# Kernel tuning notes

Hardware: AMD Instinct MI355X
Metric: run time of the kernel (lower is better)

Reference implementation:

```python
import jax, jax.numpy as jnp
import numpy as np

NG, ND, D, H = 50000, 20000, 128, 128
EGG, EGDA, ELAB = 800000, 400000, 200000
EPS, SLOPE = 1e-5, 0.01


def setup_inputs() -> dict:
    key = jax.random.key(0)
    ks = jax.random.split(key, 24)
    w = lambda k, s: jax.random.normal(k, s, jnp.float32) * 0.05
    return {
        "x_gene": jax.random.normal(ks[0], (NG, D), jnp.float32),
        "x_disease": jax.random.normal(ks[1], (ND, D), jnp.float32),
        "W_dst1": w(ks[2], (3, D, H)), "W_src1": w(ks[3], (3, D, H)),
        "W_upd1": w(ks[4], (3, 2 * H, H)),
        "b_dst1": w(ks[5], (3, H)), "b_src1": w(ks[6], (3, H)), "b_upd1": w(ks[7], (3, H)),
        "W_dst2": w(ks[8], (3, H, H)), "W_src2": w(ks[9], (3, H, H)),
        "W_upd2": w(ks[10], (3, 2 * H, H)),
        "b_dst2": w(ks[11], (3, H)), "b_src2": w(ks[12], (3, H)), "b_upd2": w(ks[13], (3, H)),
        "bn_gamma": jnp.ones((2, H), jnp.float32), "bn_beta": jnp.zeros((2, H), jnp.float32),
        "gg_src": jax.random.randint(ks[14], (EGG,), 0, NG, jnp.int32),
        "gg_dst": jax.random.randint(ks[15], (EGG,), 0, NG, jnp.int32),
        "gda_src": jax.random.randint(ks[16], (EGDA,), 0, NG, jnp.int32),
        "gda_dst": jax.random.randint(ks[17], (EGDA,), 0, ND, jnp.int32),
        "label_src": jax.random.randint(ks[18], (ELAB,), 0, NG, jnp.int32),
        "label_dst": jax.random.randint(ks[19], (ELAB,), 0, ND, jnp.int32),
    }


def _mean_agg(x_src, src_idx, dst_idx, n_dst):
    # matmul(adj_t, x_src, reduce='mean'): per-dst mean of neighbor features (0 if no in-edges)
    s = jax.ops.segment_sum(x_src[src_idx], dst_idx, num_segments=n_dst)
    deg = jax.ops.segment_sum(jnp.ones((src_idx.shape[0],), x_src.dtype), dst_idx, num_segments=n_dst)
    return s / jnp.maximum(deg, 1.0)[:, None]


def _conv(i, x_src, x_dst, src_idx, dst_idx, n_dst, Wd, Ws, Wu, bd, bs, bu):
    agg = _mean_agg(x_src, src_idx, dst_idx, n_dst)
    dst_msg = x_dst @ Wd[i] + bd[i]
    src_msg = agg @ Ws[i] + bs[i]
    return jnp.concatenate([dst_msg, src_msg], axis=1) @ Wu[i] + bu[i]


def _layer(xg, xd, Wd, Ws, Wu, bd, bs, bu, gg_src, gg_dst, gda_src, gda_dst):
    out_gg = _conv(0, xg, xg, gg_src, gg_dst, NG, Wd, Ws, Wu, bd, bs, bu)    # gene -> gene
    out_gda = _conv(1, xg, xd, gda_src, gda_dst, ND, Wd, Ws, Wu, bd, bs, bu)  # gene -> disease
    out_rev = _conv(2, xd, xg, gda_dst, gda_src, NG, Wd, Ws, Wu, bd, bs, bu)  # disease -> gene (reverse edges)
    gene = 0.5 * (out_gg + out_rev)  # stack+mean across edge types for gene dst
    return gene, out_gda


def _bn(x, g, b):
    # BatchNorm1d in training mode: batch stats over node dim, biased variance
    m = jnp.mean(x, axis=0)
    v = jnp.mean((x - m) ** 2, axis=0)
    return (x - m) * jax.lax.rsqrt(v + EPS) * g + b


def _lrelu(x):
    return jnp.where(x >= 0, x, SLOPE * x)


def reference(x_gene, x_disease, W_dst1, W_src1, W_upd1, b_dst1, b_src1, b_upd1,
              W_dst2, W_src2, W_upd2, b_dst2, b_src2, b_upd2, bn_gamma, bn_beta,
              gg_src, gg_dst, gda_src, gda_dst, label_src, label_dst):
    g, d = _layer(x_gene, x_disease, W_dst1, W_src1, W_upd1, b_dst1, b_src1, b_upd1,
                  gg_src, gg_dst, gda_src, gda_dst)
    g = _lrelu(_bn(g, bn_gamma[0], bn_beta[0]))
    d = _lrelu(_bn(d, bn_gamma[1], bn_beta[1]))
    g, d = _layer(g, d, W_dst2, W_src2, W_upd2, b_dst2, b_src2, b_upd2,
                  gg_src, gg_dst, gda_src, gda_dst)
    # dot-product decoder on supervision (gene, gda, disease) label edges
    return jnp.sum(g[label_src] * d[label_dst], axis=-1)
```

## Files before the change

### kernel.cpp

```cpp
#include <hip/hip_runtime.h>
#include <hip/hip_bf16.h>
#include <cstddef>

#define NG   50000
#define ND   20000
#define DH   128
#define EGG  800000
#define EGDA 400000
#define ELAB 200000

#define B1G 391
#define B1D 157
#define TB  939
#define TBP 940
#define PB0 0
#define PB1 (NG+1)
#define PB2 (NG+1+ND+1)

typedef __hip_bfloat16  bf16;
typedef __attribute__((ext_vector_type(8))) short bf16x8;
typedef __attribute__((ext_vector_type(4))) float f32x4;
typedef __attribute__((ext_vector_type(2))) float f32x2;

__device__ __forceinline__ float bf2f(short s){
  return __uint_as_float(((unsigned)(unsigned short)s) << 16);
}
__device__ __forceinline__ unsigned short f2b(float x){
  unsigned u = __float_as_uint(x);
  return (unsigned short)((u + 0x7FFF + ((u >> 16) & 1)) >> 16);
}

__device__ __forceinline__ float fp8_dec1(unsigned v){
  unsigned s = (v >> 7) & 1, e = (v >> 3) & 15, m = v & 7;
  float r = e ? __uint_as_float(((e + 120) << 23) | (m << 20))
              : (float)m * 0.001953125f;
  return s ? -r : r;
}
__device__ __forceinline__ unsigned fp8_enc1(float x){
  float a = fabsf(x);
  if (a > 448.f) a = 448.f;
  unsigned sgn = (__float_as_uint(x) >> 31) << 7;
  unsigned res;
  if (a < 0.015625f){
    res = (unsigned)__float2int_rn(a * 512.f);
    if (res > 7) res = 8;
    if (res == 8) res = 0x08;
  } else {
    unsigned ab = __float_as_uint(a);
    unsigned r = ab + 0x0007FFFF + ((ab >> 20) & 1);
    int e = (int)(r >> 23) - 127;
    unsigned m = (r >> 20) & 7;
    if (e > 8){ e = 8; m = 6; }
    res = ((unsigned)(e + 7) << 3) | m;
  }
  return res | sgn;
}

__device__ __forceinline__ void fp8x4_acc(unsigned w, float* a){
#if __has_builtin(__builtin_amdgcn_cvt_pk_f32_fp8)
  f32x2 p0 = __builtin_amdgcn_cvt_pk_f32_fp8((int)w, false);
  f32x2 p1 = __builtin_amdgcn_cvt_pk_f32_fp8((int)w, true);
  a[0] += p0.x; a[1] += p0.y; a[2] += p1.x; a[3] += p1.y;
#else
  a[0] += fp8_dec1(w & 255);
  a[1] += fp8_dec1((w >> 8) & 255);
  a[2] += fp8_dec1((w >> 16) & 255);
  a[3] += fp8_dec1(w >> 24);
#endif
}
__device__ __forceinline__ unsigned fp8x4_enc(float x0, float x1, float x2, float x3){
#if __has_builtin(__builtin_amdgcn_cvt_pk_fp8_f32)
  int v = 0;
  v = __builtin_amdgcn_cvt_pk_fp8_f32(x0, x1, v, false);
  v = __builtin_amdgcn_cvt_pk_fp8_f32(x2, x3, v, true);
  return (unsigned)v;
#else
  return fp8_enc1(x0) | (fp8_enc1(x1) << 8) | (fp8_enc1(x2) << 16) | (fp8_enc1(x3) << 24);
#endif
}

__global__ __launch_bounds__(256) void k_hist1(const int* __restrict__ k0, const int* __restrict__ k1,
                                               const int* __restrict__ k2, int* __restrict__ hist){
  __shared__ int lh[400];
  const int g = blockIdx.y;
  const int n  = (g == 0) ? EGG : EGDA;
  const int B1 = (g == 1) ? B1D : B1G;
  const int bb = (g == 0) ? 0 : (g == 1 ? B1G : B1G + B1D);
  const int* key = (g == 0) ? k0 : (g == 1 ? k1 : k2);
  for (int t = threadIdx.x; t < B1; t += 256) lh[t] = 0;
  __syncthreads();
  for (int i = blockIdx.x*blockDim.x + threadIdx.x; i < n; i += gridDim.x*blockDim.x)
    atomicAdd(&lh[key[i] >> 7], 1);
  __syncthreads();
  for (int t = threadIdx.x; t < B1; t += 256){
    int c = lh[t];
    if (c) atomicAdd(&hist[bb + t], c);
  }
}

__global__ __launch_bounds__(1024) void k_exscan(const int* __restrict__ cnt,
                                                 int* __restrict__ ptr, int* __restrict__ cur, int n){
  __shared__ int wsum[16];
  __shared__ int carry;
  const int tid = threadIdx.x, lane = tid & 63, wid = tid >> 6;
  if (tid == 0) carry = 0;
  __syncthreads();
  for (int base = 0; base < n; base += 4096){
    int i0 = base + tid*4;
    int4 v = {0,0,0,0};
    if (i0 < n) v = *(const int4*)(cnt + i0);
    int tsum = v.x + v.y + v.z + v.w;
    int x = tsum;
    #pragma unroll
    for (int off = 1; off < 64; off <<= 1){
      int t = __shfl_up(x, off);
      if (lane >= off) x += t;
    }
    if (lane == 63) wsum[wid] = x;
    __syncthreads();
    if (wid == 0 && lane < 16){
      int w = wsum[lane];
      #pragma unroll
      for (int off = 1; off < 16; off <<= 1){
        int t = __shfl_up(w, off);
        if (lane >= off) w += t;
      }
      wsum[lane] = w;
    }
    __syncthreads();
    int waveoff = wid ? wsum[wid-1] : 0;
    if (i0 < n){
      int ex = carry + waveoff + x - tsum;
      int4 o;
      o.x = ex; o.y = ex + v.x; o.z = o.y + v.y; o.w = o.z + v.z;
      *(int4*)(ptr + i0) = o;
      *(int4*)(cur + i0) = o;
    }
    int total = wsum[15];
    __syncthreads();
    if (tid == 0) carry += total;
    __syncthreads();
  }
  if (tid == 0) ptr[n] = carry;
}

__global__ __launch_bounds__(256) void k_scatter1(const int* __restrict__ k0, const int* __restrict__ v0,
                                                  const int* __restrict__ k1, const int* __restrict__ v1,
                                                  int* __restrict__ gcur, unsigned* __restrict__ pk){
  __shared__ int lh[400];
  __shared__ int base[400];
  const int g = blockIdx.y;
  const int n  = (g == 0) ? EGG : EGDA;
  const int B1 = (g == 1) ? B1D : B1G;
  const int bb = (g == 0) ? 0 : (g == 1 ? B1G : B1G + B1D);
  const int* key = (g == 0) ? k0 : (g == 1 ? k1 : v1);
  const int* val = (g == 0) ? v0 : (g == 1 ? v1 : k1);
  const int tid = threadIdx.x;
  const int chunk0 = blockIdx.x*4096;
  if (chunk0 >= n) return;
  for (int t = tid; t < B1; t += 256) lh[t] = 0;
  __syncthreads();
  int kd[16], vv[16];
  #pragma unroll
  for (int it = 0; it < 16; ++it){
    int i = chunk0 + it*256 + tid;
    int k = -1, v = 0;
    if (i < n){ k = key[i]; v = val[i]; atomicAdd(&lh[k >> 7], 1); }
    kd[it] = k; vv[it] = v;
  }
  __syncthreads();
  for (int t = tid; t < B1; t += 256){
    int c = lh[t];
    base[t] = c ? atomicAdd(&gcur[bb + t], c) : 0;
    lh[t] = 0;
  }
  __syncthreads();
  #pragma unroll
  for (int it = 0; it < 16; ++it){
    int k = kd[it];
    if (k >= 0){
      int b = k >> 7;
      int p = base[b] + atomicAdd(&lh[b], 1);
      pk[p] = ((unsigned)(k & 127) << 17) | (unsigned)vv[it];
    }
  }
}

__global__ __launch_bounds__(256) void k_csr2(const unsigned* __restrict__ pk,
                                              const int* __restrict__ gbase,
                                              int* __restrict__ ptr_all, int* __restrict__ col){
  __shared__ int lh[128];
  __shared__ int cur[128];
  __shared__ int sh0;
  const int b = blockIdx.x, tid = threadIdx.x;
  int lb, pbase, Ngr, bend;
  if (b < B1G)            { lb = b;             pbase = PB0; Ngr = NG; bend = B1G; }
  else if (b < B1G + B1D) { lb = b - B1G;       pbase = PB1; Ngr = ND; bend = B1G + B1D; }
  else                    { lb = b - B1G - B1D; pbase = PB2; Ngr = NG; bend = TB; }
  const int s = gbase[b], e = gbase[b+1];
  if (tid < 128) lh[tid] = 0;
  __syncthreads();
  for (int i = s + tid; i < e; i += 256)
    atomicAdd(&lh[(pk[i] >> 17) & 127], 1);
  __syncthreads();
  int lane = tid & 63;
  int v = 0, x = 0;
  if (tid < 128){
    v = lh[tid]; x = v;
    #pragma unroll
    for (int o = 1; o < 64; o <<= 1){
      int t = __shfl_up(x, o);
      if (lane >= o) x += t;
    }
    if (tid == 63) sh0 = x;
  }
  __syncthreads();
  if (tid < 128){
    int excl = x - v + (tid >= 64 ? sh0 : 0);
    cur[tid] = s + excl;
    int loc = (lb << 7) + tid;
    if (loc < Ngr) ptr_all[pbase + loc] = s + excl;
  }
  __syncthreads();
  for (int i = s + tid; i < e; i += 256){
    unsigned p = pk[i];
    int dl = (p >> 17) & 127;
    int pos = atomicAdd(&cur[dl], 1);
    col[pos] = (int)(p & 0x1FFFFu);
  }
  if (lb == 0 && tid == 0) ptr_all[pbase + Ngr] = gbase[bend];
}

#define PREP_F2B_BLOCKS (((NG+ND)*32)/256)
__global__ __launch_bounds__(256) void k_prep(
    const float* __restrict__ Wd1, const float* __restrict__ Ws1, const float* __restrict__ Wu1,
    const float* __restrict__ Wd2, const float* __restrict__ Ws2, const float* __restrict__ Wu2,
    const float* __restrict__ bd1, const float* __restrict__ bs1, const float* __restrict__ bu1,
    const float* __restrict__ bd2, const float* __restrict__ bs2, const float* __restrict__ bu2,
    float* __restrict__ AB, float* __restrict__ cv,
    const float* __restrict__ Xg, const float* __restrict__ Xd,
    unsigned short* __restrict__ Yg, unsigned short* __restrict__ Yd,
    unsigned* __restrict__ Yg8, unsigned* __restrict__ Yd8){
  const int b = blockIdx.x, tid = threadIdx.x;
  if (b < 768){
    int idx = b*256 + tid;
    int layer = idx / 98304;
    int r0 = idx - layer*98304;
    int mat = r0 >> 14;
    int r   = (r0 >> 7) & 127;
    int c   = r0 & 127;
    int i   = mat >> 1;
    int isB = mat & 1;
    const float* Wd = layer ? Wd2 : Wd1;
    const float* Ws = layer ? Ws2 : Ws1;
    const float* Wu = layer ? Wu2 : Wu1;
    const float* P = (isB ? Ws : Wd) + i*16384 + r*128;
    const float* Q = Wu + i*32768 + (isB ? 16384 : 0) + c;
    float s = 0.f;
    for (int h = 0; h < 128; ++h) s += P[h] * Q[h*128];
    AB[idx] = s;
  } else if (b < 771){
    int idx = (b - 768)*256 + tid;
    if (idx >= 768) return;
    int layer = idx / 384;
    int r = idx - layer*384;
    int i = r >> 7, h = r & 127;
    const float* bd = layer ? bd2 : bd1;
    const float* bs = layer ? bs2 : bs1;
    const float* bu = layer ? bu2 : bu1;
    const float* Wu = layer ? Wu2 : Wu1;
    float s = bu[i*128 + h];
    const float* Ut = Wu + i*32768 + h;
    const float* Ub = Ut + 16384;
    for (int k = 0; k < 128; ++k)
      s += bd[i*128 + k] * Ut[k*128] + bs[i*128 + k] * Ub[k*128];
    cv[idx] = s;
  } else {
    int idx = (b - 771)*256 + tid;
    const int GQ = NG*32;
    const float* X; unsigned short* Y; unsigned* Y8; int i;
    if (idx < GQ){ X = Xg; Y = Yg; Y8 = Yg8; i = idx; }
    else         { X = Xd; Y = Yd; Y8 = Yd8; i = idx - GQ; }
    float4 v = ((const float4*)X)[i];
    ushort4 o;
    o.x = f2b(v.x); o.y = f2b(v.y); o.z = f2b(v.z); o.w = f2b(v.w);
    ((ushort4*)Y)[i] = o;
    Y8[i] = fp8x4_enc(v.x, v.y, v.z, v.w);
  }
}

__global__ __launch_bounds__(256) void k_pack(const float* __restrict__ AB, const float* __restrict__ cv,
                                              bf16* __restrict__ Wg1, bf16* __restrict__ Wd1p,
                                              bf16* __restrict__ Wg2, bf16* __restrict__ Wd2p,
                                              float* __restrict__ cg1, float* __restrict__ cd1,
                                              float* __restrict__ cg2, float* __restrict__ cd2){
  int idx = blockIdx.x*256 + threadIdx.x;
  int layer = idx / 81920;
  int rem = idx - layer*81920;
  const float* ABl = AB + layer*98304;
  const float* cvl = cv + layer*384;
  if (rem < 49152){
    int n0  = rem / 6144;
    int r2  = rem - n0*6144;
    int ks  = r2 >> 9;
    int lane = (r2 >> 3) & 63;
    int j   = r2 & 7;
    int k   = ks*32 + (lane >> 4)*8 + j;
    int c   = n0*16 + (lane & 15);
    float v;
    if      (k < 128) v = 0.5f*(ABl[0*16384 + k*128 + c] + ABl[4*16384 + k*128 + c]);
    else if (k < 256) v = 0.5f* ABl[1*16384 + (k-128)*128 + c];
    else              v = 0.5f* ABl[5*16384 + (k-256)*128 + c];
    bf16* W = layer ? Wg2 : Wg1;
    ((unsigned short*)W)[rem] = f2b(v);
    if (rem < 128){
      float* cg = layer ? cg2 : cg1;
      cg[rem] = 0.5f*(cvl[rem] + cvl[256 + rem]);
    }
  } else {
    int d = rem - 49152;
    int n0  = d >> 12;
    int ks  = (d >> 9) & 7;
    int lane = (d >> 3) & 63;
    int j   = d & 7;
    int k   = ks*32 + (lane >> 4)*8 + j;
    int c   = n0*16 + (lane & 15);
    float v = (k < 128) ? ABl[2*16384 + k*128 + c] : ABl[3*16384 + (k-128)*128 + c];
    bf16* W = layer ? Wd2p : Wd1p;
    ((unsigned short*)W)[d] = f2b(v);
    if (d < 128){
      float* cd = layer ? cd2 : cd1;
      cd[d] = cvl[128 + d];
    }
  }
}

__global__ __launch_bounds__(256) void k_agg(const unsigned* __restrict__ Xg8, const unsigned* __restrict__ Xd8,
    const int* __restrict__ ptr_all, const int* __restrict__ col,
    bf16* __restrict__ OutGG, bf16* __restrict__ OutGDA, bf16* __restrict__ OutREV){
  int q = (blockIdx.x*256 + threadIdx.x) >> 4;
  int lane = threadIdx.x & 15;
  const unsigned* X; bf16* Out; const int* ptr; int dst;
  if (q < NG)          { X = Xg8; Out = OutGG;  ptr = ptr_all + PB0; dst = q; }
  else if (q < NG+ND)  { X = Xg8; Out = OutGDA; ptr = ptr_all + PB1; dst = q - NG; }
  else                 { X = Xd8; Out = OutREV; ptr = ptr_all + PB2; dst = q - NG - ND; }
  int s = ptr[dst], e = ptr[dst+1];
  float a[8];
  #pragma unroll
  for (int j = 0; j < 8; ++j) a[j] = 0.f;
  const int loff = lane*2;
  int i = s;
  for (; i + 4 <= e; i += 4){
    uint2 u0 = *(const uint2*)(X + (size_t)col[i  ]*32 + loff);
    uint2 u1 = *(const uint2*)(X + (size_t)col[i+1]*32 + loff);
    uint2 u2 = *(const uint2*)(X + (size_t)col[i+2]*32 + loff);
    uint2 u3 = *(const uint2*)(X + (size_t)col[i+3]*32 + loff);
    fp8x4_acc(u0.x, a);     fp8x4_acc(u0.y, a+4);
    fp8x4_acc(u1.x, a);     fp8x4_acc(u1.y, a+4);
    fp8x4_acc(u2.x, a);     fp8x4_acc(u2.y, a+4);
    fp8x4_acc(u3.x, a);     fp8x4_acc(u3.y, a+4);
  }
  for (; i < e; ++i){
    uint2 u = *(const uint2*)(X + (size_t)col[i]*32 + loff);
    fp8x4_acc(u.x, a);      fp8x4_acc(u.y, a+4);
  }
  float inv = 1.f / fmaxf((float)(e - s), 1.f);
  bf16x8 o;
  #pragma unroll
  for (int j = 0; j < 8; ++j) o[j] = (short)f2b(a[j]*inv);
  *(bf16x8*)(Out + (size_t)dst*DH + (size_t)lane*8) = o;
}

template<int KS>
__device__ __forceinline__ void gemm_body(
    const bf16* __restrict__ X0, const bf16* __restrict__ X1, const bf16* __restrict__ X2,
    const bf16* __restrict__ Wp, const float* __restrict__ cvec,
    unsigned short* __restrict__ Out, int M, int blk){
  const int tid = threadIdx.x;
  const int wave = tid >> 6, lane = tid & 63;
  const int lrow = lane & 15, quad = lane >> 4;
  const int row0 = blk*32;
  const bf16* Xs[3] = {X0, X1, X2};
  f32x4 acc[2][2];
  #pragma unroll
  for (int p = 0; p < 2; ++p)
    #pragma unroll
    for (int t = 0; t < 2; ++t) acc[p][t] = 0.0f;
  const bf16x8* wp = (const bf16x8*)Wp;
  const int f00 = (2*wave*KS)*64 + lane;
  #pragma unroll
  for (int ks = 0; ks < KS; ++ks){
    const bf16* Xm = Xs[ks >> 2];
    const int kk = (ks & 3)*32 + quad*8;
    bf16x8 a[2];
    #pragma unroll
    for (int t = 0; t < 2; ++t){
      int ar = row0 + t*16 + lrow; if (ar > M-1) ar = M-1;
      a[t] = *(const bf16x8*)(Xm + (size_t)ar*DH + kk);
    }
    bf16x8 b0 = wp[f00 + ks*64];
    bf16x8 b1 = wp[f00 + (KS + ks)*64];
    #pragma unroll
    for (int t = 0; t < 2; ++t){
      acc[0][t] = __builtin_amdgcn_mfma_f32_16x16x32_bf16(a[t], b0, acc[0][t], 0, 0, 0);
      acc[1][t] = __builtin_amdgcn_mfma_f32_16x16x32_bf16(a[t], b1, acc[1][t], 0, 0, 0);
    }
  }
  #pragma unroll
  for (int p = 0; p < 2; ++p){
    int c = (2*wave + p)*16 + lrow;
    float cb = cvec[c];
    #pragma unroll
    for (int t = 0; t < 2; ++t){
      #pragma unroll
      for (int r = 0; r < 4; ++r){
        int row = row0 + t*16 + quad*4 + r;
        if (row < M) Out[(size_t)row*DH + c] = f2b(acc[p][t][r] + cb);
      }
    }
  }
}

#define GBGENE ((NG+31)/32)
#define GBDIS  ((ND+31)/32)

__global__ __launch_bounds__(256) void k_gemm(
    const bf16* __restrict__ Xg, const bf16* __restrict__ Ag, const bf16* __restrict__ Rg,
    const bf16* __restrict__ Wg, const float* __restrict__ cg, unsigned short* __restrict__ Og,
    const bf16* __restrict__ Xd, const bf16* __restrict__ Ad,
    const bf16* __restrict__ Wd, const float* __restrict__ cd, unsigned short* __restrict__ Od){
  if ((int)blockIdx.x < GBGENE)
    gemm_body<12>(Xg, Ag, Rg, Wg, cg, Og, NG, blockIdx.x);
  else
    gemm_body<8>(Xd, Ad, Ad, Wd, cd, Od, ND, blockIdx.x - GBGENE);
}

#define SBG 192
#define SBD 64
__global__ __launch_bounds__(256) void k_bn_stats(const bf16* __restrict__ Xgb, const bf16* __restrict__ Xdb,
                                                  float* __restrict__ sums){
  __shared__ float acc[256];
  int tid = threadIdx.x;
  acc[tid] = 0.f;
  __syncthreads();
  int g = (int)blockIdx.x >= SBG;
  int bidx = blockIdx.x - (g ? SBG : 0);
  int NB = g ? SBD : SBG;
  int N  = g ? ND : NG;
  const bf16* Xb = g ? Xdb : Xgb;
  float* sm = sums + g*256;
  int c8 = (tid & 15)*8;
  int rl = tid >> 4;
  float s[8], q[8];
  #pragma unroll
  for (int j = 0; j < 8; ++j){ s[j] = 0.f; q[j] = 0.f; }
  for (int r = bidx*16 + rl; r < N; r += NB*16){
    bf16x8 v = *(const bf16x8*)(Xb + (size_t)r*DH + c8);
    #pragma unroll
    for (int j = 0; j < 8; ++j){
      float f = bf2f(v[j]);
      s[j] += f; q[j] += f*f;
    }
  }
  #pragma unroll
  for (int j = 0; j < 8; ++j){
    atomicAdd(&acc[c8+j], s[j]);
    atomicAdd(&acc[128+c8+j], q[j]);
  }
  __syncthreads();
  atomicAdd(&sm[tid], acc[tid]);
}

__global__ __launch_bounds__(256) void k_bn_apply(const bf16* __restrict__ Xgb, const bf16* __restrict__ Xdb,
    const float* __restrict__ sums, const float* __restrict__ gamma, const float* __restrict__ beta,
    unsigned short* __restrict__ Yg, unsigned short* __restrict__ Yd,
    uint2* __restrict__ Yg8, uint2* __restrict__ Yd8){
  __shared__ float sc[256], sb[256];
  int tid = threadIdx.x;
  {
    int g = tid >> 7, c = tid & 127;
    float invN = g ? (1.f/ND) : (1.f/NG);
    const float* sm = sums + g*256;
    float m = sm[c]*invN;
    float v = sm[128 + c]*invN - m*m;
    float s = rsqrtf(v + 1e-5f) * gamma[g*128 + c];
    sc[tid] = s;
    sb[tid] = beta[g*128 + c] - m*s;
  }
  __syncthreads();
  const int GT = NG*16;
  const int TOT = GT + ND*16;
  for (int idx = blockIdx.x*256 + tid; idx < TOT; idx += gridDim.x*256){
    const bf16x8* src; bf16x8* dst; uint2* dst8; int i, cb;
    if (idx < GT){ src = (const bf16x8*)Xgb; dst = (bf16x8*)Yg; dst8 = Yg8; i = idx; cb = 0; }
    else         { src = (const bf16x8*)Xdb; dst = (bf16x8*)Yd; dst8 = Yd8; i = idx - GT; cb = 128; }
    bf16x8 v = src[i];
    int c = cb + (i & 15)*8;
    float y[8];
    bf16x8 o;
    #pragma unroll
    for (int j = 0; j < 8; ++j){
      float t = bf2f(v[j])*sc[c+j] + sb[c+j];
      t = t >= 0.f ? t : 0.01f*t;
      y[j] = t;
      o[j] = (short)f2b(t);
    }
    dst[i] = o;
    uint2 p;
    p.x = fp8x4_enc(y[0], y[1], y[2], y[3]);
    p.y = fp8x4_enc(y[4], y[5], y[6], y[7]);
    dst8[i] = p;
  }
}

__global__ __launch_bounds__(256) void k_decode(const bf16* __restrict__ G, const bf16* __restrict__ Dd,
    const int* __restrict__ ls, const int* __restrict__ ld, float* __restrict__ out, int E){
  int p = (blockIdx.x*256 + threadIdx.x) >> 4;
  int lane = threadIdx.x & 15;
  int e0 = p*2, e1 = p*2 + 1;
  if (e0 >= E) return;
  int a0 = ls[e0], b0 = ld[e0];
  int a1 = ls[e1], b1 = ld[e1];
  const size_t loff = (size_t)lane*8;
  bf16x8 g0 = *(const bf16x8*)(G  + (size_t)a0*DH + loff);
  bf16x8 d0 = *(const bf16x8*)(Dd + (size_t)b0*DH + loff);
  bf16x8 g1 = *(const bf16x8*)(G  + (size_t)a1*DH + loff);
  bf16x8 d1 = *(const bf16x8*)(Dd + (size_t)b1*DH + loff);
  float s0 = 0.f, s1 = 0.f;
  #pragma unroll
  for (int j = 0; j < 8; ++j){
    s0 += bf2f(g0[j])*bf2f(d0[j]);
    s1 += bf2f(g1[j])*bf2f(d1[j]);
  }
  #pragma unroll
  for (int off = 8; off; off >>= 1){
    s0 += __shfl_down(s0, off, 16);
    s1 += __shfl_down(s1, off, 16);
  }
  if (lane == 0){ out[e0] = s0; out[e1] = s1; }
}

extern "C" void kernel_launch(void* const* d_in, const int* in_sizes, int n_in,
                              void* d_out, int out_size, void* d_ws, size_t ws_size,
                              hipStream_t stream){
  const float* x_gene = (const float*)d_in[0];
  const float* x_dis  = (const float*)d_in[1];
  const float* Wd1 = (const float*)d_in[2];
  const float* Ws1 = (const float*)d_in[3];
  const float* Wu1 = (const float*)d_in[4];
  const float* bd1 = (const float*)d_in[5];
  const float* bs1 = (const float*)d_in[6];
  const float* bu1 = (const float*)d_in[7];
  const float* Wd2 = (const float*)d_in[8];
  const float* Ws2 = (const float*)d_in[9];
  const float* Wu2 = (const float*)d_in[10];
  const float* bd2 = (const float*)d_in[11];
  const float* bs2 = (const float*)d_in[12];
  const float* bu2 = (const float*)d_in[13];
  const float* bng = (const float*)d_in[14];
  const float* bnb = (const float*)d_in[15];
  const int* gg_src  = (const int*)d_in[16];
  const int* gg_dst  = (const int*)d_in[17];
  const int* gda_src = (const int*)d_in[18];
  const int* gda_dst = (const int*)d_in[19];
  const int* lsrc = (const int*)d_in[20];
  const int* ldst = (const int*)d_in[21];

  char* ws = (char*)d_ws;
  size_t off = 0;
  auto alloc = [&](size_t bytes)->void*{
    void* p = ws + off; off += (bytes + 255) & ~(size_t)255; return p;
  };
  int* hist    = (int*)alloc(960*4);
  float* bnsum = (float*)alloc(2*256*4);
  int* gbase   = (int*)alloc(960*4);
  int* gcur    = (int*)alloc(960*4);
  int* ptr_all = (int*)alloc((size_t)(NG+1+ND+1+NG+1)*4);
  int* col     = (int*)alloc((size_t)(EGG+2*EGDA)*4);
  unsigned* pk = (unsigned*)alloc((size_t)(EGG+2*EGDA)*4);
  float* AB  = (float*)alloc(2*98304*4);
  float* cv  = (float*)alloc(2*384*4);
  float* cg1 = (float*)alloc(128*4);
  float* cd1 = (float*)alloc(128*4);
  float* cg2 = (float*)alloc(128*4);
  float* cd2 = (float*)alloc(128*4);
  bf16* Wg1  = (bf16*)alloc(49152*2);
  bf16* Wp1  = (bf16*)alloc(32768*2);
  bf16* Wg2  = (bf16*)alloc(49152*2);
  bf16* Wp2  = (bf16*)alloc(32768*2);
  bf16* xgb  = (bf16*)alloc((size_t)NG*DH*2);
  bf16* xdb  = (bf16*)alloc((size_t)ND*DH*2);
  unsigned* xg8  = (unsigned*)alloc((size_t)NG*DH);
  unsigned* xd8  = (unsigned*)alloc((size_t)ND*DH);
  unsigned* Xg28 = (unsigned*)alloc((size_t)NG*DH);
  unsigned* Xd28 = (unsigned*)alloc((size_t)ND*DH);
  bf16* aggGGb  = (bf16*)alloc((size_t)NG*DH*2);
  bf16* aggREVb = (bf16*)alloc((size_t)NG*DH*2);
  bf16* aggGDAb = (bf16*)alloc((size_t)ND*DH*2);
  bf16* Xg2b = (bf16*)alloc((size_t)NG*DH*2);
  bf16* Xd2b = (bf16*)alloc((size_t)ND*DH*2);
  bf16* outgb = (bf16*)alloc((size_t)NG*DH*2);
  bf16* outdb = (bf16*)alloc((size_t)ND*DH*2);

  hipMemsetAsync(hist, 0, 960*4 + 512*4, stream);

  {
    dim3 gh(96, 3);
    k_hist1<<<gh,256,0,stream>>>(gg_dst, gda_dst, gda_src, hist);
    k_exscan<<<1,1024,0,stream>>>(hist, gbase, gcur, TBP);
    dim3 gs(196, 3);
    k_scatter1<<<gs,256,0,stream>>>(gg_dst, gg_src, gda_dst, gda_src, gcur, pk);
    k_csr2<<<TB,256,0,stream>>>(pk, gbase, ptr_all, col);
  }

  k_prep<<<771 + PREP_F2B_BLOCKS,256,0,stream>>>(
      Wd1, Ws1, Wu1, Wd2, Ws2, Wu2, bd1, bs1, bu1, bd2, bs2, bu2,
      AB, cv, x_gene, x_dis, (unsigned short*)xgb, (unsigned short*)xdb, xg8, xd8);
  k_pack<<<640,256,0,stream>>>(AB, cv, Wg1, Wp1, Wg2, Wp2, cg1, cd1, cg2, cd2);

  k_agg<<<(NG+ND+NG)*16/256,256,0,stream>>>(xg8, xd8, ptr_all, col, aggGGb, aggGDAb, aggREVb);
  k_gemm<<<GBGENE+GBDIS,256,0,stream>>>(xgb, aggGGb, aggREVb, Wg1, cg1, (unsigned short*)outgb,
                                        xdb, aggGDAb, Wp1, cd1, (unsigned short*)outdb);
  k_bn_stats<<<SBG+SBD,256,0,stream>>>(outgb, outdb, bnsum);
  k_bn_apply<<<1024,256,0,stream>>>(outgb, outdb, bnsum, bng, bnb,
                                    (unsigned short*)Xg2b, (unsigned short*)Xd2b,
                                    (uint2*)Xg28, (uint2*)Xd28);

  k_agg<<<(NG+ND+NG)*16/256,256,0,stream>>>(Xg28, Xd28, ptr_all, col, aggGGb, aggGDAb, aggREVb);
  k_gemm<<<GBGENE+GBDIS,256,0,stream>>>(Xg2b, aggGGb, aggREVb, Wg2, cg2, (unsigned short*)outgb,
                                        Xd2b, aggGDAb, Wp2, cd2, (unsigned short*)outdb);

  k_decode<<<ELAB*16/2/256,256,0,stream>>>(outgb, outdb, lsrc, ldst, (float*)d_out, ELAB);
}
```

Baseline: 344.4 us.

## Fuse neighbor aggregation and BN statistics into the per-layer GEMM kernel

Merges the aggregation kernel, the GEMM kernel and the BN-statistics kernel into one k_layer kernel. Each 32-row block first gathers mean-aggregated neighbor features into LDS, then runs the MFMA GEMM reading aggregated operands from LDS. In the first layer it also accumulates per-column sum and sum of squares in the epilogue. This removes the global round trip for the aggregation buffers and two kernel launches per layer. In exchange, the gather work is now serialized with the GEMM inside each block, using only 16 row-gathers in flight per block, and every block issues global atomics.

Result: slower. 355.7 us (+3.3%).

```diff
diff --git a/kernel.cpp b/kernel.cpp
--- a/kernel.cpp
+++ b/kernel.cpp
@@ -335,52 +335,63 @@
   }
 }
 
-__global__ __launch_bounds__(256) void k_agg(const unsigned* __restrict__ Xg8, const unsigned* __restrict__ Xd8,
-    const int* __restrict__ ptr_all, const int* __restrict__ col,
-    bf16* __restrict__ OutGG, bf16* __restrict__ OutGDA, bf16* __restrict__ OutREV){
-  int q = (blockIdx.x*256 + threadIdx.x) >> 4;
-  int lane = threadIdx.x & 15;
-  const unsigned* X; bf16* Out; const int* ptr; int dst;
-  if (q < NG)          { X = Xg8; Out = OutGG;  ptr = ptr_all + PB0; dst = q; }
-  else if (q < NG+ND)  { X = Xg8; Out = OutGDA; ptr = ptr_all + PB1; dst = q - NG; }
-  else                 { X = Xd8; Out = OutREV; ptr = ptr_all + PB2; dst = q - NG - ND; }
-  int s = ptr[dst], e = ptr[dst+1];
-  float a[8];
-  #pragma unroll
-  for (int j = 0; j < 8; ++j) a[j] = 0.f;
-  const int loff = lane*2;
-  int i = s;
-  for (; i + 4 <= e; i += 4){
-    uint2 u0 = *(const uint2*)(X + (size_t)col[i  ]*32 + loff);
-    uint2 u1 = *(const uint2*)(X + (size_t)col[i+1]*32 + loff);
-    uint2 u2 = *(const uint2*)(X + (size_t)col[i+2]*32 + loff);
-    uint2 u3 = *(const uint2*)(X + (size_t)col[i+3]*32 + loff);
-    fp8x4_acc(u0.x, a);     fp8x4_acc(u0.y, a+4);
-    fp8x4_acc(u1.x, a);     fp8x4_acc(u1.y, a+4);
-    fp8x4_acc(u2.x, a);     fp8x4_acc(u2.y, a+4);
-    fp8x4_acc(u3.x, a);     fp8x4_acc(u3.y, a+4);
-  }
-  for (; i < e; ++i){
-    uint2 u = *(const uint2*)(X + (size_t)col[i]*32 + loff);
-    fp8x4_acc(u.x, a);      fp8x4_acc(u.y, a+4);
-  }
-  float inv = 1.f / fmaxf((float)(e - s), 1.f);
-  bf16x8 o;
-  #pragma unroll
-  for (int j = 0; j < 8; ++j) o[j] = (short)f2b(a[j]*inv);
-  *(bf16x8*)(Out + (size_t)dst*DH + (size_t)lane*8) = o;
-}
-
-template<int KS>
-__device__ __forceinline__ void gemm_body(
-    const bf16* __restrict__ X0, const bf16* __restrict__ X1, const bf16* __restrict__ X2,
+#define GBG32 ((NG+31)/32)
+#define GBD32 ((ND+31)/32)
+
+template<int KS, int DO_BN>
+__device__ __forceinline__ void layer_body(
+    const bf16* __restrict__ X0,
+    const unsigned* __restrict__ S8a, const unsigned* __restrict__ S8b,
+    const int* __restrict__ ptrA, const int* __restrict__ ptrB,
+    const int* __restrict__ col,
     const bf16* __restrict__ Wp, const float* __restrict__ cvec,
-    unsigned short* __restrict__ Out, int M, int blk){
+    unsigned short* __restrict__ Out, float* __restrict__ bnglob,
+    int M, int blk, short (*lds_agg)[32][128], float* bnacc){
   const int tid = threadIdx.x;
+  const int row0 = blk*32;
+
+  {
+    const int qw = tid >> 4, lane = tid & 15;
+    const int loff = lane*2;
+    const int NT = (KS == 12) ? 64 : 32;
+    for (int t = qw; t < NT; t += 16){
+      int lr  = (KS == 12) ? (t >> 1) : t;
+      int row = row0 + lr;
+      if (row < M){
+        int g = (KS == 12) ? (t & 1) : 0;
+        const unsigned* X8 = g ? S8b : S8a;
+        const int* ptr = g ? ptrB : ptrA;
+        int s = ptr[row], e = ptr[row+1];
+        float a[8];
+        #pragma unroll
+        for (int j = 0; j < 8; ++j) a[j] = 0.f;
+        int i = s;
+        for (; i + 4 <= e; i += 4){
+          uint2 u0 = *(const uint2*)(X8 + (size_t)col[i  ]*32 + loff);
+          uint2 u1 = *(const uint2*)(X8 + (size_t)col[i+1]*32 + loff);
+          uint2 u2 = *(const uint2*)(X8 + (size_t)col[i+2]*32 + loff);
+          uint2 u3 = *(const uint2*)(X8 + (size_t)col[i+3]*32 + loff);
+          fp8x4_acc(u0.x, a);     fp8x4_acc(u0.y, a+4);
+          fp8x4_acc(u1.x, a);     fp8x4_acc(u1.y, a+4);
+          fp8x4_acc(u2.x, a);     fp8x4_acc(u2.y, a+4);
+          fp8x4_acc(u3.x, a);     fp8x4_acc(u3.y, a+4);
+        }
+        for (; i < e; ++i){
+          uint2 u = *(const uint2*)(X8 + (size_t)col[i]*32 + loff);
+          fp8x4_acc(u.x, a);      fp8x4_acc(u.y, a+4);
+        }
+        float inv = 1.f / fmaxf((float)(e - s), 1.f);
+        bf16x8 o;
+        #pragma unroll
+        for (int j = 0; j < 8; ++j) o[j] = (short)f2b(a[j]*inv);
+        *(bf16x8*)&lds_agg[g][lr][lane*8] = o;
+      }
+    }
+  }
+  __syncthreads();
+
   const int wave = tid >> 6, lane = tid & 63;
   const int lrow = lane & 15, quad = lane >> 4;
-  const int row0 = blk*32;
-  const bf16* Xs[3] = {X0, X1, X2};
   f32x4 acc[2][2];
   #pragma unroll
   for (int p = 0; p < 2; ++p)
@@ -390,13 +401,13 @@
   const int f00 = (2*wave*KS)*64 + lane;
   #pragma unroll
   for (int ks = 0; ks < KS; ++ks){
-    const bf16* Xm = Xs[ks >> 2];
     const int kk = (ks & 3)*32 + quad*8;
     bf16x8 a[2];
     #pragma unroll
     for (int t = 0; t < 2; ++t){
       int ar = row0 + t*16 + lrow; if (ar > M-1) ar = M-1;
-      a[t] = *(const bf16x8*)(Xm + (size_t)ar*DH + kk);
+      if (ks < 4) a[t] = *(const bf16x8*)(X0 + (size_t)ar*DH + kk);
+      else        a[t] = *(const bf16x8*)&lds_agg[(ks >> 2) - 1][ar - row0][kk];
     }
     bf16x8 b0 = wp[f00 + ks*64];
     bf16x8 b1 = wp[f00 + (KS + ks)*64];
@@ -406,69 +417,55 @@
       acc[1][t] = __builtin_amdgcn_mfma_f32_16x16x32_bf16(a[t], b1, acc[1][t], 0, 0, 0);
     }
   }
+
   #pragma unroll
   for (int p = 0; p < 2; ++p){
     int c = (2*wave + p)*16 + lrow;
     float cb = cvec[c];
+    float sl = 0.f, ql = 0.f;
     #pragma unroll
     for (int t = 0; t < 2; ++t){
       #pragma unroll
       for (int r = 0; r < 4; ++r){
         int row = row0 + t*16 + quad*4 + r;
-        if (row < M) Out[(size_t)row*DH + c] = f2b(acc[p][t][r] + cb);
+        if (row < M){
+          unsigned short us = f2b(acc[p][t][r] + cb);
+          Out[(size_t)row*DH + c] = us;
+          if (DO_BN){
+            float f = bf2f((short)us);
+            sl += f; ql += f*f;
+          }
+        }
       }
     }
-  }
-}
-
-#define GBGENE ((NG+31)/32)
-#define GBDIS  ((ND+31)/32)
-
-__global__ __launch_bounds__(256) void k_gemm(
-    const bf16* __restrict__ Xg, const bf16* __restrict__ Ag, const bf16* __restrict__ Rg,
+    if (DO_BN){
+      atomicAdd(&bnacc[c], sl);
+      atomicAdd(&bnacc[128 + c], ql);
+    }
+  }
+  if (DO_BN){
+    __syncthreads();
+    atomicAdd(&bnglob[tid], bnacc[tid]);
+  }
+}
+
+template<int DO_BN>
+__global__ __launch_bounds__(256) void k_layer(
+    const bf16* __restrict__ Xg, const bf16* __restrict__ Xd,
+    const unsigned* __restrict__ xg8, const unsigned* __restrict__ xd8,
+    const int* __restrict__ ptr_all, const int* __restrict__ col,
     const bf16* __restrict__ Wg, const float* __restrict__ cg, unsigned short* __restrict__ Og,
-    const bf16* __restrict__ Xd, const bf16* __restrict__ Ad,
-    const bf16* __restrict__ Wd, const float* __restrict__ cd, unsigned short* __restrict__ Od){
-  if ((int)blockIdx.x < GBGENE)
-    gemm_body<12>(Xg, Ag, Rg, Wg, cg, Og, NG, blockIdx.x);
+    const bf16* __restrict__ Wd, const float* __restrict__ cd, unsigned short* __restrict__ Od,
+    float* __restrict__ bnsum){
+  __shared__ short lds_agg[2][32][128];
+  __shared__ float bnacc[256];
+  if (DO_BN) bnacc[threadIdx.x] = 0.f;
+  if ((int)blockIdx.x < GBG32)
+    layer_body<12, DO_BN>(Xg, xg8, xd8, ptr_all + PB0, ptr_all + PB2, col,
+                          Wg, cg, Og, bnsum, NG, blockIdx.x, lds_agg, bnacc);
   else
-    gemm_body<8>(Xd, Ad, Ad, Wd, cd, Od, ND, blockIdx.x - GBGENE);
-}
-
-#define SBG 192
-#define SBD 64
-__global__ __launch_bounds__(256) void k_bn_stats(const bf16* __restrict__ Xgb, const bf16* __restrict__ Xdb,
-                                                  float* __restrict__ sums){
-  __shared__ float acc[256];
-  int tid = threadIdx.x;
-  acc[tid] = 0.f;
-  __syncthreads();
-  int g = (int)blockIdx.x >= SBG;
-  int bidx = blockIdx.x - (g ? SBG : 0);
-  int NB = g ? SBD : SBG;
-  int N  = g ? ND : NG;
-  const bf16* Xb = g ? Xdb : Xgb;
-  float* sm = sums + g*256;
-  int c8 = (tid & 15)*8;
-  int rl = tid >> 4;
-  float s[8], q[8];
-  #pragma unroll
-  for (int j = 0; j < 8; ++j){ s[j] = 0.f; q[j] = 0.f; }
-  for (int r = bidx*16 + rl; r < N; r += NB*16){
-    bf16x8 v = *(const bf16x8*)(Xb + (size_t)r*DH + c8);
-    #pragma unroll
-    for (int j = 0; j < 8; ++j){
-      float f = bf2f(v[j]);
-      s[j] += f; q[j] += f*f;
-    }
-  }
-  #pragma unroll
-  for (int j = 0; j < 8; ++j){
-    atomicAdd(&acc[c8+j], s[j]);
-    atomicAdd(&acc[128+c8+j], q[j]);
-  }
-  __syncthreads();
-  atomicAdd(&sm[tid], acc[tid]);
+    layer_body<8, DO_BN>(Xd, xg8, xg8, ptr_all + PB1, ptr_all + PB1, col,
+                         Wd, cd, Od, bnsum + 256, ND, blockIdx.x - GBG32, lds_agg, bnacc);
 }
 
 __global__ __launch_bounds__(256) void k_bn_apply(const bf16* __restrict__ Xgb, const bf16* __restrict__ Xdb,
@@ -594,9 +591,6 @@
   unsigned* xd8  = (unsigned*)alloc((size_t)ND*DH);
   unsigned* Xg28 = (unsigned*)alloc((size_t)NG*DH);
   unsigned* Xd28 = (unsigned*)alloc((size_t)ND*DH);
-  bf16* aggGGb  = (bf16*)alloc((size_t)NG*DH*2);
-  bf16* aggREVb = (bf16*)alloc((size_t)NG*DH*2);
-  bf16* aggGDAb = (bf16*)alloc((size_t)ND*DH*2);
   bf16* Xg2b = (bf16*)alloc((size_t)NG*DH*2);
   bf16* Xd2b = (bf16*)alloc((size_t)ND*DH*2);
   bf16* outgb = (bf16*)alloc((size_t)NG*DH*2);
@@ -618,17 +612,16 @@
       AB, cv, x_gene, x_dis, (unsigned short*)xgb, (unsigned short*)xdb, xg8, xd8);
   k_pack<<<640,256,0,stream>>>(AB, cv, Wg1, Wp1, Wg2, Wp2, cg1, cd1, cg2, cd2);
 
-  k_agg<<<(NG+ND+NG)*16/256,256,0,stream>>>(xg8, xd8, ptr_all, col, aggGGb, aggGDAb, aggREVb);
-  k_gemm<<<GBGENE+GBDIS,256,0,stream>>>(xgb, aggGGb, aggREVb, Wg1, cg1, (unsigned short*)outgb,
-                                        xdb, aggGDAb, Wp1, cd1, (unsigned short*)outdb);
-  k_bn_stats<<<SBG+SBD,256,0,stream>>>(outgb, outdb, bnsum);
+  k_layer<1><<<GBG32+GBD32,256,0,stream>>>(xgb, xdb, xg8, xd8, ptr_all, col,
+                                           Wg1, cg1, (unsigned short*)outgb,
+                                           Wp1, cd1, (unsigned short*)outdb, bnsum);
   k_bn_apply<<<1024,256,0,stream>>>(outgb, outdb, bnsum, bng, bnb,
                                     (unsigned short*)Xg2b, (unsigned short*)Xd2b,
                                     (uint2*)Xg28, (uint2*)Xd28);
 
-  k_agg<<<(NG+ND+NG)*16/256,256,0,stream>>>(Xg28, Xd28, ptr_all, col, aggGGb, aggGDAb, aggREVb);
-  k_gemm<<<GBGENE+GBDIS,256,0,stream>>>(Xg2b, aggGGb, aggREVb, Wg2, cg2, (unsigned short*)outgb,
-                                        Xd2b, aggGDAb, Wp2, cd2, (unsigned short*)outdb);
+  k_layer<0><<<GBG32+GBD32,256,0,stream>>>(Xg2b, Xd2b, Xg28, Xd28, ptr_all, col,
+                                           Wg2, cg2, (unsigned short*)outgb,
+                                           Wp2, cd2, (unsigned short*)outdb, bnsum);
 
   k_decode<<<ELAB*16/2/256,256,0,stream>>>(outgb, outdb, lsrc, ldst, (float*)d_out, ELAB);
 }
```

## Replace histogram+scan CSR build with fixed-capacity per-bucket slots

Applied to the files above, without the earlier changes.

Removes the histogram and exclusive-scan kernels by giving each 128-destination bucket a fixed 4096-entry slot region and using atomic bucket counters directly as offsets. Per-destination CSR pointers become (start,count) pairs so the sparse layout needs no global prefix. This saves two kernel launches and a pass over the edge keys, but relies on no bucket exceeding the capacity and spreads edge storage over a larger, gapped region.

Result: faster. 329.9 us (-4.2%).

```diff
diff --git a/kernel.cpp b/kernel.cpp
--- a/kernel.cpp
+++ b/kernel.cpp
@@ -12,10 +12,10 @@
 #define B1G 391
 #define B1D 157
 #define TB  939
-#define TBP 940
-#define PB0 0
-#define PB1 (NG+1)
-#define PB2 (NG+1+ND+1)
+#define CAP 4096
+#define SE0 0
+#define SE1 NG
+#define SE2 (NG+ND)
 
 typedef __hip_bfloat16  bf16;
 typedef __attribute__((ext_vector_type(8))) short bf16x8;
@@ -79,71 +79,6 @@
 #endif
 }
 
-__global__ __launch_bounds__(256) void k_hist1(const int* __restrict__ k0, const int* __restrict__ k1,
-                                               const int* __restrict__ k2, int* __restrict__ hist){
-  __shared__ int lh[400];
-  const int g = blockIdx.y;
-  const int n  = (g == 0) ? EGG : EGDA;
-  const int B1 = (g == 1) ? B1D : B1G;
-  const int bb = (g == 0) ? 0 : (g == 1 ? B1G : B1G + B1D);
-  const int* key = (g == 0) ? k0 : (g == 1 ? k1 : k2);
-  for (int t = threadIdx.x; t < B1; t += 256) lh[t] = 0;
-  __syncthreads();
-  for (int i = blockIdx.x*blockDim.x + threadIdx.x; i < n; i += gridDim.x*blockDim.x)
-    atomicAdd(&lh[key[i] >> 7], 1);
-  __syncthreads();
-  for (int t = threadIdx.x; t < B1; t += 256){
-    int c = lh[t];
-    if (c) atomicAdd(&hist[bb + t], c);
-  }
-}
-
-__global__ __launch_bounds__(1024) void k_exscan(const int* __restrict__ cnt,
-                                                 int* __restrict__ ptr, int* __restrict__ cur, int n){
-  __shared__ int wsum[16];
-  __shared__ int carry;
-  const int tid = threadIdx.x, lane = tid & 63, wid = tid >> 6;
-  if (tid == 0) carry = 0;
-  __syncthreads();
-  for (int base = 0; base < n; base += 4096){
-    int i0 = base + tid*4;
-    int4 v = {0,0,0,0};
-    if (i0 < n) v = *(const int4*)(cnt + i0);
-    int tsum = v.x + v.y + v.z + v.w;
-    int x = tsum;
-    #pragma unroll
-    for (int off = 1; off < 64; off <<= 1){
-      int t = __shfl_up(x, off);
-      if (lane >= off) x += t;
-    }
-    if (lane == 63) wsum[wid] = x;
-    __syncthreads();
-    if (wid == 0 && lane < 16){
-      int w = wsum[lane];
-      #pragma unroll
-      for (int off = 1; off < 16; off <<= 1){
-        int t = __shfl_up(w, off);
-        if (lane >= off) w += t;
-      }
-      wsum[lane] = w;
-    }
-    __syncthreads();
-    int waveoff = wid ? wsum[wid-1] : 0;
-    if (i0 < n){
-      int ex = carry + waveoff + x - tsum;
-      int4 o;
-      o.x = ex; o.y = ex + v.x; o.z = o.y + v.y; o.w = o.z + v.z;
-      *(int4*)(ptr + i0) = o;
-      *(int4*)(cur + i0) = o;
-    }
-    int total = wsum[15];
-    __syncthreads();
-    if (tid == 0) carry += total;
-    __syncthreads();
-  }
-  if (tid == 0) ptr[n] = carry;
-}
-
 __global__ __launch_bounds__(256) void k_scatter1(const int* __restrict__ k0, const int* __restrict__ v0,
                                                   const int* __restrict__ k1, const int* __restrict__ v1,
                                                   int* __restrict__ gcur, unsigned* __restrict__ pk){
@@ -171,7 +106,7 @@
   __syncthreads();
   for (int t = tid; t < B1; t += 256){
     int c = lh[t];
-    base[t] = c ? atomicAdd(&gcur[bb + t], c) : 0;
+    base[t] = c ? ((bb + t)*CAP + atomicAdd(&gcur[bb + t], c)) : 0;
     lh[t] = 0;
   }
   __syncthreads();
@@ -187,17 +122,17 @@
 }
 
 __global__ __launch_bounds__(256) void k_csr2(const unsigned* __restrict__ pk,
-                                              const int* __restrict__ gbase,
-                                              int* __restrict__ ptr_all, int* __restrict__ col){
+                                              const int* __restrict__ gcur,
+                                              int2* __restrict__ se_all, int* __restrict__ col){
   __shared__ int lh[128];
   __shared__ int cur[128];
   __shared__ int sh0;
   const int b = blockIdx.x, tid = threadIdx.x;
-  int lb, pbase, Ngr, bend;
-  if (b < B1G)            { lb = b;             pbase = PB0; Ngr = NG; bend = B1G; }
-  else if (b < B1G + B1D) { lb = b - B1G;       pbase = PB1; Ngr = ND; bend = B1G + B1D; }
-  else                    { lb = b - B1G - B1D; pbase = PB2; Ngr = NG; bend = TB; }
-  const int s = gbase[b], e = gbase[b+1];
+  int lb, sbase, Ngr;
+  if (b < B1G)            { lb = b;             sbase = SE0; Ngr = NG; }
+  else if (b < B1G + B1D) { lb = b - B1G;       sbase = SE1; Ngr = ND; }
+  else                    { lb = b - B1G - B1D; sbase = SE2; Ngr = NG; }
+  const int s = b*CAP, e = s + gcur[b];
   if (tid < 128) lh[tid] = 0;
   __syncthreads();
   for (int i = s + tid; i < e; i += 256)
@@ -219,7 +154,7 @@
     int excl = x - v + (tid >= 64 ? sh0 : 0);
     cur[tid] = s + excl;
     int loc = (lb << 7) + tid;
-    if (loc < Ngr) ptr_all[pbase + loc] = s + excl;
+    if (loc < Ngr) se_all[sbase + loc] = make_int2(s + excl, v);
   }
   __syncthreads();
   for (int i = s + tid; i < e; i += 256){
@@ -228,7 +163,6 @@
     int pos = atomicAdd(&cur[dl], 1);
     col[pos] = (int)(p & 0x1FFFFu);
   }
-  if (lb == 0 && tid == 0) ptr_all[pbase + Ngr] = gbase[bend];
 }
 
 #define PREP_F2B_BLOCKS (((NG+ND)*32)/256)
@@ -336,15 +270,16 @@
 }
 
 __global__ __launch_bounds__(256) void k_agg(const unsigned* __restrict__ Xg8, const unsigned* __restrict__ Xd8,
-    const int* __restrict__ ptr_all, const int* __restrict__ col,
+    const int2* __restrict__ se_all, const int* __restrict__ col,
     bf16* __restrict__ OutGG, bf16* __restrict__ OutGDA, bf16* __restrict__ OutREV){
   int q = (blockIdx.x*256 + threadIdx.x) >> 4;
   int lane = threadIdx.x & 15;
-  const unsigned* X; bf16* Out; const int* ptr; int dst;
-  if (q < NG)          { X = Xg8; Out = OutGG;  ptr = ptr_all + PB0; dst = q; }
-  else if (q < NG+ND)  { X = Xg8; Out = OutGDA; ptr = ptr_all + PB1; dst = q - NG; }
-  else                 { X = Xd8; Out = OutREV; ptr = ptr_all + PB2; dst = q - NG - ND; }
-  int s = ptr[dst], e = ptr[dst+1];
+  const unsigned* X; bf16* Out; const int2* se; int dst;
+  if (q < NG)          { X = Xg8; Out = OutGG;  se = se_all + SE0; dst = q; }
+  else if (q < NG+ND)  { X = Xg8; Out = OutGDA; se = se_all + SE1; dst = q - NG; }
+  else                 { X = Xd8; Out = OutREV; se = se_all + SE2; dst = q - NG - ND; }
+  int2 sd = se[dst];
+  int s = sd.x, e = sd.x + sd.y;
   float a[8];
   #pragma unroll
   for (int j = 0; j < 8; ++j) a[j] = 0.f;
@@ -571,13 +506,11 @@
   auto alloc = [&](size_t bytes)->void*{
     void* p = ws + off; off += (bytes + 255) & ~(size_t)255; return p;
   };
-  int* hist    = (int*)alloc(960*4);
+  int* gcur    = (int*)alloc(960*4);
   float* bnsum = (float*)alloc(2*256*4);
-  int* gbase   = (int*)alloc(960*4);
-  int* gcur    = (int*)alloc(960*4);
-  int* ptr_all = (int*)alloc((size_t)(NG+1+ND+1+NG+1)*4);
-  int* col     = (int*)alloc((size_t)(EGG+2*EGDA)*4);
-  unsigned* pk = (unsigned*)alloc((size_t)(EGG+2*EGDA)*4);
+  int2* se_all = (int2*)alloc((size_t)(NG+ND+NG)*8);
+  int* col     = (int*)alloc((size_t)TB*CAP*4);
+  unsigned* pk = (unsigned*)alloc((size_t)TB*CAP*4);
   float* AB  = (float*)alloc(2*98304*4);
   float* cv  = (float*)alloc(2*384*4);
   float* cg1 = (float*)alloc(128*4);
@@ -602,15 +535,12 @@
   bf16* outgb = (bf16*)alloc((size_t)NG*DH*2);
   bf16* outdb = (bf16*)alloc((size_t)ND*DH*2);
 
-  hipMemsetAsync(hist, 0, 960*4 + 512*4, stream);
+  hipMemsetAsync(gcur, 0, 960*4 + 512*4, stream);
 
   {
-    dim3 gh(96, 3);
-    k_hist1<<<gh,256,0,stream>>>(gg_dst, gda_dst, gda_src, hist);
-    k_exscan<<<1,1024,0,stream>>>(hist, gbase, gcur, TBP);
     dim3 gs(196, 3);
     k_scatter1<<<gs,256,0,stream>>>(gg_dst, gg_src, gda_dst, gda_src, gcur, pk);
-    k_csr2<<<TB,256,0,stream>>>(pk, gbase, ptr_all, col);
+    k_csr2<<<TB,256,0,stream>>>(pk, gcur, se_all, col);
   }
 
   k_prep<<<771 + PREP_F2B_BLOCKS,256,0,stream>>>(
@@ -618,7 +548,7 @@
       AB, cv, x_gene, x_dis, (unsigned short*)xgb, (unsigned short*)xdb, xg8, xd8);
   k_pack<<<640,256,0,stream>>>(AB, cv, Wg1, Wp1, Wg2, Wp2, cg1, cd1, cg2, cd2);
 
-  k_agg<<<(NG+ND+NG)*16/256,256,0,stream>>>(xg8, xd8, ptr_all, col, aggGGb, aggGDAb, aggREVb);
+  k_agg<<<(NG+ND+NG)*16/256,256,0,stream>>>(xg8, xd8, se_all, col, aggGGb, aggGDAb, aggREVb);
   k_gemm<<<GBGENE+GBDIS,256,0,stream>>>(xgb, aggGGb, aggREVb, Wg1, cg1, (unsigned short*)outgb,
                                         xdb, aggGDAb, Wp1, cd1, (unsigned short*)outdb);
   k_bn_stats<<<SBG+SBD,256,0,stream>>>(outgb, outdb, bnsum);
@@ -626,7 +556,7 @@
                                     (unsigned short*)Xg2b, (unsigned short*)Xd2b,
                                     (uint2*)Xg28, (uint2*)Xd28);
 
-  k_agg<<<(NG+ND+NG)*16/256,256,0,stream>>>(Xg28, Xd28, ptr_all, col, aggGGb, aggGDAb, aggREVb);
+  k_agg<<<(NG+ND+NG)*16/256,256,0,stream>>>(Xg28, Xd28, se_all, col, aggGGb, aggGDAb, aggREVb);
   k_gemm<<<GBGENE+GBDIS,256,0,stream>>>(Xg2b, aggGGb, aggREVb, Wg2, cg2, (unsigned short*)outgb,
                                         Xd2b, aggGDAb, Wp2, cd2, (unsigned short*)outdb);
 
```
